# Kernel tuning notes

Hardware: AMD Instinct MI355X
Metric: run time of the kernel (lower is better)

The kernel has to match this reference:

```python
import jax, jax.numpy as jnp
import numpy as np

NEG_SLOPE = 0.01  # nn.LeakyReLU default


def setup_inputs() -> dict:
    key = jax.random.key(0)
    k1, k2, k3, k4, k5 = jax.random.split(key, 5)
    SLI, FEAT, NODE = 8, 64, 20000
    N = SLI * NODE          # 160000 graph nodes
    E = 2_560_000           # avg degree 16
    OUT = 64
    inputs = jax.random.normal(k1, (SLI, FEAT, NODE), dtype=jnp.float32)
    src = jax.random.randint(k2, (E,), 0, N, dtype=jnp.int64)
    dst = jax.random.randint(k3, (E,), 0, N, dtype=jnp.int64)
    # GraphConv params (glorot-ish scale)
    W = jax.random.normal(k4, (FEAT, OUT), dtype=jnp.float32) / np.sqrt(FEAT)
    b = jnp.zeros((OUT,), dtype=jnp.float32)
    return {"inputs": inputs, "W": W, "b": b, "src": src, "dst": dst}


def reference(inputs, W, b, src, dst):
    # inputs: [sli, feat, node] -> [sli*node, feat]  (dropout is eval-mode identity)
    sli, feat, node = inputs.shape
    x = jnp.transpose(inputs, (0, 2, 1)).reshape(-1, feat)
    N = sli * node
    ones = jnp.ones(src.shape, dtype=x.dtype)
    deg_out = jax.ops.segment_sum(ones, src, num_segments=N)  # out-degree of src
    deg_in = jax.ops.segment_sum(ones, dst, num_segments=N)   # in-degree of dst
    norm_src = jnp.where(deg_out > 0, deg_out, 1.0) ** -0.5
    norm_dst = jnp.where(deg_in > 0, deg_in, 1.0) ** -0.5
    # norm='both': scale src feats, sum-aggregate over edges, scale dst
    h = x * norm_src[:, None]
    agg = jax.ops.segment_sum(h[src], dst, num_segments=N)    # [N, feat]
    agg = agg * norm_dst[:, None]
    out = agg @ W + b                                          # [N, out]
    out = jax.nn.leaky_relu(out, NEG_SLOPE)
    # [N, out] -> [sli, node, out] -> [sli, out, node]
    return jnp.transpose(out.reshape(sli, node, -1), (0, 2, 1))
```

## Files before the change

kernel.cpp:

```cpp
#include <hip/hip_runtime.h>
#include <hip/hip_bf16.h>

constexpr int SLI  = 8;
constexpr int FEAT = 64;
constexpr int NODE = 20000;
constexpr int NTOT = SLI * NODE;
constexpr int OUTF = 64;
constexpr int CAP  = 48;
constexpr int NB   = 313;
constexpr int BCAP = 8960;
constexpr int EPB  = 4096;
constexpr int NDST = NTOT / 256;

typedef __attribute__((ext_vector_type(8))) short bf16x8;
typedef __attribute__((ext_vector_type(4))) float f32x4;

static __device__ inline unsigned short f2bf(float x) {
    unsigned u = __float_as_uint(x);
    unsigned r = (u + 0x7fffu + ((u >> 16) & 1u)) >> 16;
    return (unsigned short)r;
}
static __device__ inline float bf2f(unsigned short h) {
    return __uint_as_float((unsigned)h << 16);
}

__global__ __launch_bounds__(256) void k_part(const int* __restrict__ src,
                                              const int* __restrict__ dst,
                                              int* __restrict__ cursor_d,
                                              unsigned* __restrict__ bucket_d,
                                              int* __restrict__ cursor_s,
                                              unsigned short* __restrict__ bucket_s, int E) {
    __shared__ unsigned       svalD[EPB];
    __shared__ unsigned short sbktD[EPB];
    __shared__ unsigned short svalS[EPB];
    __shared__ unsigned short sbktS[EPB];
    __shared__ int histD[NB], loffD[NB], lcurD[NB], baseD[NB];
    __shared__ int histS[NB], loffS[NB], lcurS[NB], baseS[NB];
    __shared__ int goffD[64], goffS[64];
    int t  = threadIdx.x;
    int e0 = blockIdx.x * EPB;
    for (int i = t; i < NB; i += 256) { histD[i] = 0; histS[i] = 0; }
    __syncthreads();
    int myS[16], myD[16];
#pragma unroll
    for (int i = 0; i < 16; ++i) {
        int idx = e0 + i * 256 + t;
        if (idx < E) {
            myS[i] = src[idx];
            myD[i] = dst[idx];
            atomicAdd(&histD[myD[i] >> 9], 1);
            atomicAdd(&histS[myS[i] >> 9], 1);
        } else { myS[i] = -1; myD[i] = -1; }
    }
    __syncthreads();
    int wv = t >> 6, ln = t & 63;
    if (wv == 0) {
        int b0 = ln * 5, s = 0;
#pragma unroll
        for (int j = 0; j < 5; ++j) { int bb = b0 + j; if (bb < NB) s += histD[bb]; }
        int x = s;
        for (int off = 1; off < 64; off <<= 1) {
            int y = __shfl_up(x, off, 64);
            if (ln >= off) x += y;
        }
        goffD[ln] = x - s;
    } else if (wv == 1) {
        int b0 = ln * 5, s = 0;
#pragma unroll
        for (int j = 0; j < 5; ++j) { int bb = b0 + j; if (bb < NB) s += histS[bb]; }
        int x = s;
        for (int off = 1; off < 64; off <<= 1) {
            int y = __shfl_up(x, off, 64);
            if (ln >= off) x += y;
        }
        goffS[ln] = x - s;
    }
    __syncthreads();
    for (int bb = t; bb < NB; bb += 256) {
        int g5 = bb / 5;
        int sD = goffD[g5], sS = goffS[g5];
        for (int k = g5 * 5; k < bb; ++k) { sD += histD[k]; sS += histS[k]; }
        loffD[bb] = sD; lcurD[bb] = sD;
        baseD[bb] = atomicAdd(&cursor_d[bb], histD[bb]);
        loffS[bb] = sS; lcurS[bb] = sS;
        baseS[bb] = atomicAdd(&cursor_s[bb], histS[bb]);
    }
    __syncthreads();
#pragma unroll
    for (int i = 0; i < 16; ++i) {
        if (myD[i] >= 0) {
            int bD = myD[i] >> 9;
            int p  = atomicAdd(&lcurD[bD], 1);
            svalD[p] = ((unsigned)(myD[i] & 511) << 18) | (unsigned)myS[i];
            sbktD[p] = (unsigned short)bD;
            int bS = myS[i] >> 9;
            int q  = atomicAdd(&lcurS[bS], 1);
            svalS[q] = (unsigned short)(myS[i] & 511);
            sbktS[q] = (unsigned short)bS;
        }
    }
    __syncthreads();
    int nval = E - e0; if (nval > EPB) nval = EPB;
    for (int p = t; p < nval; p += 256) {
        int bD = sbktD[p];
        int wi = baseD[bD] + (p - loffD[bD]);
        if (wi < BCAP) bucket_d[(size_t)bD * BCAP + wi] = svalD[p];
        int bS = sbktS[p];
        int wj = baseS[bS] + (p - loffS[bS]);
        if (wj < BCAP) bucket_s[(size_t)bS * BCAP + wj] = svalS[p];
    }
}

__global__ __launch_bounds__(256) void k_fin(const int* __restrict__ cursor_d,
                                             const unsigned* __restrict__ bucket_d,
                                             const int* __restrict__ cursor_s,
                                             const unsigned short* __restrict__ bucket_s,
                                             int* __restrict__ col_ell,
                                             int* __restrict__ deg_in,
                                             int* __restrict__ deg_out) {
    __shared__ char lds[256 * CAP * 4 + 2048];
    int t = threadIdx.x;
    if (blockIdx.x < NDST) {
        int* ell = (int*)lds;
        int* cnt = (int*)(lds + 256 * CAP * 4);
        int blk  = blockIdx.x, b = blk >> 1, half = blk & 1;
        cnt[t] = 0;
        __syncthreads();
        int len = cursor_d[b]; if (len > BCAP) len = BCAP;
        const unsigned* p = bucket_d + (size_t)b * BCAP;
        for (int i = t; i < len; i += 256) {
            unsigned e = p[i];
            int dl = e >> 18;
            if ((dl >> 8) == half) {
                int r = dl & 255;
                int pos = atomicAdd(&cnt[r], 1);
                if (pos < CAP) ell[r * CAP + pos] = (int)(e & 0x3FFFFu);
            }
        }
        __syncthreads();
        int node0 = blk << 8;
        deg_in[node0 + t] = cnt[t];
        size_t gbase = (size_t)node0 * CAP;
        const int4* lsrc = (const int4*)ell;
        int4* gdst = (int4*)(col_ell + gbase);
#pragma unroll
        for (int i = 0; i < 12; ++i)
            gdst[i * 256 + t] = lsrc[i * 256 + t];
    } else {
        int* cnt = (int*)lds;
        int b = blockIdx.x - NDST;
        cnt[t] = 0; cnt[t + 256] = 0;
        __syncthreads();
        int len = cursor_s[b]; if (len > BCAP) len = BCAP;
        const unsigned short* p = bucket_s + (size_t)b * BCAP;
        for (int i = t; i < len; i += 256)
            atomicAdd(&cnt[p[i]], 1);
        __syncthreads();
        int n0 = b << 9;
        if (n0 + t < NTOT)       deg_out[n0 + t] = cnt[t];
        if (n0 + 256 + t < NTOT) deg_out[n0 + 256 + t] = cnt[t + 256];
    }
}

__global__ __launch_bounds__(256) void k_transpose(const float* __restrict__ in,
                                                   const int* __restrict__ deg_out,
                                                   __hip_bfloat16* __restrict__ xs) {
    __shared__ float tile[64][65];
    int sli = blockIdx.y;
    int n0  = blockIdx.x * 64;
    int t   = threadIdx.x;
    int tx  = t & 63;
    int tr  = t >> 6;
    const float* ip = in + (size_t)sli * FEAT * NODE;
#pragma unroll
    for (int i = 0; i < 16; ++i) {
        int f    = tr + i * 4;
        int node = n0 + tx;
        float v  = 0.f;
        if (node < NODE) v = ip[(size_t)f * NODE + node];
        tile[f][tx] = v;
    }
    __syncthreads();
#pragma unroll
    for (int i = 0; i < 16; ++i) {
        int nl   = tr + i * 4;
        int node = n0 + nl;
        if (node < NODE) {
            int n = sli * NODE + node;
            int d = deg_out[n];
            float scale = rsqrtf(d > 0 ? (float)d : 1.f);
            xs[(size_t)n * FEAT + tx] = (__hip_bfloat16)(tile[tx][nl] * scale);
        }
    }
}

__global__ __launch_bounds__(256) void k_agg_gemm(const int* __restrict__ deg_in,
                                                  const int* __restrict__ col_ell,
                                                  const unsigned short* __restrict__ xs,
                                                  const float* __restrict__ W,
                                                  const float* __restrict__ b,
                                                  float* __restrict__ out) {
    __shared__ char lds[27648];
    unsigned short* av_hi = (unsigned short*)lds;
    unsigned short* av_lo = (unsigned short*)(lds + 9216);
    unsigned short* wt    = (unsigned short*)(lds + 18432);
    float (*otile)[65]    = (float(*)[65])lds;

    int t    = threadIdx.x;
    int lane = t & 63;
    int w    = t >> 6;
    int gq   = lane >> 4;
    int fl   = lane & 15;
    int sli  = blockIdx.y;
    int n0   = blockIdx.x * 64;

#pragma unroll
    for (int i = 0; i < 16; ++i) {
        int idx = i * 256 + t;
        int f = idx >> 6, o = idx & 63;
        wt[o * 72 + f] = f2bf(W[idx]);
    }

    int m0 = w * 16;
    for (int ii = 0; ii < 16; ii += 2) {
        int rowA = m0 + ii, rowB = rowA + 1;
        int nodeA = n0 + rowA, nodeB = n0 + rowB;
        int nA = sli * NODE + nodeA, nB = sli * NODE + nodeB;
        int dA = (nodeA < NODE) ? deg_in[nA] : 0;
        int dB = (nodeB < NODE) ? deg_in[nB] : 0;
        int degA = dA < CAP ? dA : CAP;
        int degB = dB < CAP ? dB : CAP;
        int cA = (lane < degA) ? col_ell[(size_t)nA * CAP + lane] : 0;
        int cB = (lane < degB) ? col_ell[(size_t)nB * CAP + lane] : 0;
        float a0 = 0.f, a1 = 0.f, a2 = 0.f, a3 = 0.f;
        float b0 = 0.f, b1 = 0.f, b2 = 0.f, b3 = 0.f;
        int gmax = degA > degB ? degA : degB;
        int groups = (gmax + 3) >> 2;
        for (int j = 0; j < groups; ++j) {
            int idx = 4 * j + gq;
            int sA = __shfl(cA, idx, 64);
            int sB = __shfl(cB, idx, 64);
            uint2 vA = *(const uint2*)(xs + (size_t)sA * 64 + fl * 4);
            uint2 vB = *(const uint2*)(xs + (size_t)sB * 64 + fl * 4);
            if (idx < degA) {
                a0 += __uint_as_float(vA.x << 16);
                a1 += __uint_as_float(vA.x & 0xffff0000u);
                a2 += __uint_as_float(vA.y << 16);
                a3 += __uint_as_float(vA.y & 0xffff0000u);
            }
            if (idx < degB) {
                b0 += __uint_as_float(vB.x << 16);
                b1 += __uint_as_float(vB.x & 0xffff0000u);
                b2 += __uint_as_float(vB.y << 16);
                b3 += __uint_as_float(vB.y & 0xffff0000u);
            }
        }
        a0 += __shfl_xor(a0, 16, 64); a0 += __shfl_xor(a0, 32, 64);
        a1 += __shfl_xor(a1, 16, 64); a1 += __shfl_xor(a1, 32, 64);
        a2 += __shfl_xor(a2, 16, 64); a2 += __shfl_xor(a2, 32, 64);
        a3 += __shfl_xor(a3, 16, 64); a3 += __shfl_xor(a3, 32, 64);
        b0 += __shfl_xor(b0, 16, 64); b0 += __shfl_xor(b0, 32, 64);
        b1 += __shfl_xor(b1, 16, 64); b1 += __shfl_xor(b1, 32, 64);
        b2 += __shfl_xor(b2, 16, 64); b2 += __shfl_xor(b2, 32, 64);
        b3 += __shfl_xor(b3, 16, 64); b3 += __shfl_xor(b3, 32, 64);
        if (gq == 0) {
            float scA = rsqrtf(dA > 0 ? (float)dA : 1.f);
            float scB = rsqrtf(dB > 0 ? (float)dB : 1.f);
            float s0 = a0 * scA, s1 = a1 * scA, s2 = a2 * scA, s3 = a3 * scA;
            float u0 = b0 * scB, u1 = b1 * scB, u2 = b2 * scB, u3 = b3 * scB;
            unsigned short h0 = f2bf(s0), h1 = f2bf(s1), h2 = f2bf(s2), h3 = f2bf(s3);
            uint2 hv, lv;
            hv.x = (unsigned)h0 | ((unsigned)h1 << 16);
            hv.y = (unsigned)h2 | ((unsigned)h3 << 16);
            lv.x = (unsigned)f2bf(s0 - bf2f(h0)) | ((unsigned)f2bf(s1 - bf2f(h1)) << 16);
            lv.y = (unsigned)f2bf(s2 - bf2f(h2)) | ((unsigned)f2bf(s3 - bf2f(h3)) << 16);
            ((uint2*)av_hi)[rowA * 18 + fl] = hv;
            ((uint2*)av_lo)[rowA * 18 + fl] = lv;
            unsigned short g0 = f2bf(u0), g1 = f2bf(u1), g2 = f2bf(u2), g3 = f2bf(u3);
            hv.x = (unsigned)g0 | ((unsigned)g1 << 16);
            hv.y = (unsigned)g2 | ((unsigned)g3 << 16);
            lv.x = (unsigned)f2bf(u0 - bf2f(g0)) | ((unsigned)f2bf(u1 - bf2f(g1)) << 16);
            lv.y = (unsigned)f2bf(u2 - bf2f(g2)) | ((unsigned)f2bf(u3 - bf2f(g3)) << 16);
            ((uint2*)av_hi)[rowB * 18 + fl] = hv;
            ((uint2*)av_lo)[rowB * 18 + fl] = lv;
        }
    }

    __syncthreads();

    int q = lane >> 4, r16 = lane & 15;
    bf16x8 a_hi[2], a_lo[2], bfr[4][2];
#pragma unroll
    for (int ks = 0; ks < 2; ++ks) {
        a_hi[ks] = *(const bf16x8*)(av_hi + (m0 + r16) * 72 + ks * 32 + q * 8);
        a_lo[ks] = *(const bf16x8*)(av_lo + (m0 + r16) * 72 + ks * 32 + q * 8);
    }
#pragma unroll
    for (int nt = 0; nt < 4; ++nt)
#pragma unroll
        for (int ks = 0; ks < 2; ++ks)
            bfr[nt][ks] = *(const bf16x8*)(wt + (nt * 16 + r16) * 72 + ks * 32 + q * 8);

    f32x4 acc4[4];
#pragma unroll
    for (int nt = 0; nt < 4; ++nt) acc4[nt] = (f32x4){0.f, 0.f, 0.f, 0.f};
#pragma unroll
    for (int nt = 0; nt < 4; ++nt)
#pragma unroll
        for (int ks = 0; ks < 2; ++ks) {
            acc4[nt] = __builtin_amdgcn_mfma_f32_16x16x32_bf16(a_hi[ks], bfr[nt][ks], acc4[nt], 0, 0, 0);
            acc4[nt] = __builtin_amdgcn_mfma_f32_16x16x32_bf16(a_lo[ks], bfr[nt][ks], acc4[nt], 0, 0, 0);
        }
    __syncthreads();

#pragma unroll
    for (int nt = 0; nt < 4; ++nt) {
        int oc = nt * 16 + r16;
        float bias = b[oc];
#pragma unroll
        for (int r = 0; r < 4; ++r) {
            float v = acc4[nt][r] + bias;
            v = v > 0.f ? v : 0.01f * v;
            otile[oc][m0 + q * 4 + r] = v;
        }
    }
    __syncthreads();

    const size_t obase = (size_t)sli * OUTF * NODE;
#pragma unroll
    for (int i = 0; i < 16; ++i) {
        int o    = w + i * 4;
        int node = n0 + lane;
        if (node < NODE)
            out[obase + (size_t)o * NODE + node] = otile[o][lane];
    }
}

extern "C" void kernel_launch(void* const* d_in, const int* in_sizes, int n_in,
                              void* d_out, int out_size, void* d_ws, size_t ws_size,
                              hipStream_t stream) {
    const float* inputs = (const float*)d_in[0];
    const float* W      = (const float*)d_in[1];
    const float* b      = (const float*)d_in[2];
    const int*   src    = (const int*)d_in[3];
    const int*   dst    = (const int*)d_in[4];
    float*       out    = (float*)d_out;
    const int E = in_sizes[3];

    char* ws = (char*)d_ws;
    int* deg_out = (int*)ws;
    int* deg_in  = (int*)(ws + (size_t)NTOT * 4);
    int* col_ell = (int*)(ws + (size_t)2 * NTOT * 4);
    char* R      = (char*)col_ell + (size_t)NTOT * CAP * 4;
    unsigned*       bucket_d = (unsigned*)R;
    unsigned short* bucket_s = (unsigned short*)(R + (size_t)NB * BCAP * 4);
    int*            cursors  = (int*)(R + (size_t)NB * BCAP * 6);
    int* cursor_d = cursors;
    int* cursor_s = cursors + NB;
    __hip_bfloat16* xs = (__hip_bfloat16*)R;

    hipMemsetAsync(cursors, 0, (size_t)2 * NB * 4, stream);

    int PB = (E + EPB - 1) / EPB;
    k_part<<<PB, 256, 0, stream>>>(src, dst, cursor_d, bucket_d, cursor_s, bucket_s, E);

    k_fin<<<NDST + NB, 256, 0, stream>>>(cursor_d, bucket_d, cursor_s, bucket_s,
                                         col_ell, deg_in, deg_out);

    dim3 tgrid((NODE + 63) / 64, SLI);
    k_transpose<<<tgrid, 256, 0, stream>>>(inputs, deg_out, xs);

    k_agg_gemm<<<tgrid, 256, 0, stream>>>(deg_in, col_ell,
                                          (const unsigned short*)xs, W, b, out);
}
```

Before: 261.4 us.

## Drop hi/lo bf16 split, widen gather loads, vectorize transpose, pack partition LDS

The aggregation GEMM now uses a single bf16 operand instead of the hi+lo split, which halves the MFMA work and A-tile LDS traffic but loses the extra precision the split provided. The gather loop reads 16 bytes per lane over 8 edges per iteration. Padded lanes point at a zero row at index NTOT (cleared by a memset) instead of using per-edge predicates. The transpose kernel uses float4 loads and packed bf16x2 stores, and the partition kernel merges the src value and bucket into one 32-bit LDS word.

```diff
diff --git a/kernel.cpp b/kernel.cpp
--- a/kernel.cpp
+++ b/kernel.cpp
@@ -20,9 +20,6 @@
     unsigned r = (u + 0x7fffu + ((u >> 16) & 1u)) >> 16;
     return (unsigned short)r;
 }
-static __device__ inline float bf2f(unsigned short h) {
-    return __uint_as_float((unsigned)h << 16);
-}
 
 __global__ __launch_bounds__(256) void k_part(const int* __restrict__ src,
                                               const int* __restrict__ dst,
@@ -32,8 +29,7 @@
                                               unsigned short* __restrict__ bucket_s, int E) {
     __shared__ unsigned       svalD[EPB];
     __shared__ unsigned short sbktD[EPB];
-    __shared__ unsigned short svalS[EPB];
-    __shared__ unsigned short sbktS[EPB];
+    __shared__ unsigned       sS[EPB];
     __shared__ int histD[NB], loffD[NB], lcurD[NB], baseD[NB];
     __shared__ int histS[NB], loffS[NB], lcurS[NB], baseS[NB];
     __shared__ int goffD[64], goffS[64];
@@ -78,11 +74,11 @@
     __syncthreads();
     for (int bb = t; bb < NB; bb += 256) {
         int g5 = bb / 5;
-        int sD = goffD[g5], sS = goffS[g5];
-        for (int k = g5 * 5; k < bb; ++k) { sD += histD[k]; sS += histS[k]; }
+        int sD = goffD[g5], sS2 = goffS[g5];
+        for (int k = g5 * 5; k < bb; ++k) { sD += histD[k]; sS2 += histS[k]; }
         loffD[bb] = sD; lcurD[bb] = sD;
         baseD[bb] = atomicAdd(&cursor_d[bb], histD[bb]);
-        loffS[bb] = sS; lcurS[bb] = sS;
+        loffS[bb] = sS2; lcurS[bb] = sS2;
         baseS[bb] = atomicAdd(&cursor_s[bb], histS[bb]);
     }
     __syncthreads();
@@ -95,8 +91,7 @@
             sbktD[p] = (unsigned short)bD;
             int bS = myS[i] >> 9;
             int q  = atomicAdd(&lcurS[bS], 1);
-            svalS[q] = (unsigned short)(myS[i] & 511);
-            sbktS[q] = (unsigned short)bS;
+            sS[q] = ((unsigned)bS << 9) | (unsigned)(myS[i] & 511);
         }
     }
     __syncthreads();
@@ -105,9 +100,10 @@
         int bD = sbktD[p];
         int wi = baseD[bD] + (p - loffD[bD]);
         if (wi < BCAP) bucket_d[(size_t)bD * BCAP + wi] = svalD[p];
-        int bS = sbktS[p];
+        unsigned vs = sS[p];
+        int bS = vs >> 9;
         int wj = baseS[bS] + (p - loffS[bS]);
-        if (wj < BCAP) bucket_s[(size_t)bS * BCAP + wj] = svalS[p];
+        if (wj < BCAP) bucket_s[(size_t)bS * BCAP + wj] = (unsigned short)(vs & 511);
     }
 }
 
@@ -164,32 +160,39 @@
 
 __global__ __launch_bounds__(256) void k_transpose(const float* __restrict__ in,
                                                    const int* __restrict__ deg_out,
-                                                   __hip_bfloat16* __restrict__ xs) {
+                                                   unsigned short* __restrict__ xs) {
     __shared__ float tile[64][65];
     int sli = blockIdx.y;
     int n0  = blockIdx.x * 64;
     int t   = threadIdx.x;
-    int tx  = t & 63;
-    int tr  = t >> 6;
+    int fx  = t & 15;
+    int fr  = t >> 4;
     const float* ip = in + (size_t)sli * FEAT * NODE;
-#pragma unroll
-    for (int i = 0; i < 16; ++i) {
-        int f    = tr + i * 4;
-        int node = n0 + tx;
-        float v  = 0.f;
-        if (node < NODE) v = ip[(size_t)f * NODE + node];
-        tile[f][tx] = v;
-    }
-    __syncthreads();
-#pragma unroll
-    for (int i = 0; i < 16; ++i) {
-        int nl   = tr + i * 4;
+    int nq = n0 + fx * 4;
+#pragma unroll
+    for (int i = 0; i < 4; ++i) {
+        int f = fr + i * 16;
+        float4 v = {0.f, 0.f, 0.f, 0.f};
+        if (nq < NODE) v = *(const float4*)(ip + (size_t)f * NODE + nq);
+        tile[f][fx * 4 + 0] = v.x;
+        tile[f][fx * 4 + 1] = v.y;
+        tile[f][fx * 4 + 2] = v.z;
+        tile[f][fx * 4 + 3] = v.w;
+    }
+    __syncthreads();
+    int h  = t & 31;
+    int nr = t >> 5;
+#pragma unroll
+    for (int i = 0; i < 8; ++i) {
+        int nl   = nr + i * 8;
         int node = n0 + nl;
         if (node < NODE) {
             int n = sli * NODE + node;
             int d = deg_out[n];
-            float scale = rsqrtf(d > 0 ? (float)d : 1.f);
-            xs[(size_t)n * FEAT + tx] = (__hip_bfloat16)(tile[tx][nl] * scale);
+            float sc = rsqrtf(d > 0 ? (float)d : 1.f);
+            unsigned lo = f2bf(tile[2 * h][nl] * sc);
+            unsigned hi = f2bf(tile[2 * h + 1][nl] * sc);
+            *(unsigned*)(xs + (size_t)n * 64 + 2 * h) = lo | (hi << 16);
         }
     }
 }
@@ -200,17 +203,16 @@
                                                   const float* __restrict__ W,
                                                   const float* __restrict__ b,
                                                   float* __restrict__ out) {
-    __shared__ char lds[27648];
-    unsigned short* av_hi = (unsigned short*)lds;
-    unsigned short* av_lo = (unsigned short*)(lds + 9216);
-    unsigned short* wt    = (unsigned short*)(lds + 18432);
-    float (*otile)[65]    = (float(*)[65])lds;
+    __shared__ char lds[18432];
+    unsigned short* av = (unsigned short*)lds;
+    unsigned short* wt = (unsigned short*)(lds + 9216);
+    float (*otile)[65] = (float(*)[65])lds;
 
     int t    = threadIdx.x;
     int lane = t & 63;
     int w    = t >> 6;
-    int gq   = lane >> 4;
-    int fl   = lane & 15;
+    int g8   = lane >> 3;
+    int f8   = lane & 7;
     int sli  = blockIdx.y;
     int n0   = blockIdx.x * 64;
 
@@ -230,71 +232,68 @@
         int dB = (nodeB < NODE) ? deg_in[nB] : 0;
         int degA = dA < CAP ? dA : CAP;
         int degB = dB < CAP ? dB : CAP;
-        int cA = (lane < degA) ? col_ell[(size_t)nA * CAP + lane] : 0;
-        int cB = (lane < degB) ? col_ell[(size_t)nB * CAP + lane] : 0;
-        float a0 = 0.f, a1 = 0.f, a2 = 0.f, a3 = 0.f;
-        float b0 = 0.f, b1 = 0.f, b2 = 0.f, b3 = 0.f;
+        int cA = (lane < degA) ? col_ell[(size_t)nA * CAP + lane] : NTOT;
+        int cB = (lane < degB) ? col_ell[(size_t)nB * CAP + lane] : NTOT;
+        float accA[8] = {0,0,0,0,0,0,0,0};
+        float accB[8] = {0,0,0,0,0,0,0,0};
         int gmax = degA > degB ? degA : degB;
-        int groups = (gmax + 3) >> 2;
+        int groups = (gmax + 7) >> 3;
         for (int j = 0; j < groups; ++j) {
-            int idx = 4 * j + gq;
+            int idx = 8 * j + g8;
             int sA = __shfl(cA, idx, 64);
             int sB = __shfl(cB, idx, 64);
-            uint2 vA = *(const uint2*)(xs + (size_t)sA * 64 + fl * 4);
-            uint2 vB = *(const uint2*)(xs + (size_t)sB * 64 + fl * 4);
-            if (idx < degA) {
-                a0 += __uint_as_float(vA.x << 16);
-                a1 += __uint_as_float(vA.x & 0xffff0000u);
-                a2 += __uint_as_float(vA.y << 16);
-                a3 += __uint_as_float(vA.y & 0xffff0000u);
-            }
-            if (idx < degB) {
-                b0 += __uint_as_float(vB.x << 16);
-                b1 += __uint_as_float(vB.x & 0xffff0000u);
-                b2 += __uint_as_float(vB.y << 16);
-                b3 += __uint_as_float(vB.y & 0xffff0000u);
-            }
-        }
-        a0 += __shfl_xor(a0, 16, 64); a0 += __shfl_xor(a0, 32, 64);
-        a1 += __shfl_xor(a1, 16, 64); a1 += __shfl_xor(a1, 32, 64);
-        a2 += __shfl_xor(a2, 16, 64); a2 += __shfl_xor(a2, 32, 64);
-        a3 += __shfl_xor(a3, 16, 64); a3 += __shfl_xor(a3, 32, 64);
-        b0 += __shfl_xor(b0, 16, 64); b0 += __shfl_xor(b0, 32, 64);
-        b1 += __shfl_xor(b1, 16, 64); b1 += __shfl_xor(b1, 32, 64);
-        b2 += __shfl_xor(b2, 16, 64); b2 += __shfl_xor(b2, 32, 64);
-        b3 += __shfl_xor(b3, 16, 64); b3 += __shfl_xor(b3, 32, 64);
-        if (gq == 0) {
+            uint4 vA = *(const uint4*)(xs + (size_t)sA * 64 + f8 * 8);
+            uint4 vB = *(const uint4*)(xs + (size_t)sB * 64 + f8 * 8);
+            accA[0] += __uint_as_float(vA.x << 16);
+            accA[1] += __uint_as_float(vA.x & 0xffff0000u);
+            accA[2] += __uint_as_float(vA.y << 16);
+            accA[3] += __uint_as_float(vA.y & 0xffff0000u);
+            accA[4] += __uint_as_float(vA.z << 16);
+            accA[5] += __uint_as_float(vA.z & 0xffff0000u);
+            accA[6] += __uint_as_float(vA.w << 16);
+            accA[7] += __uint_as_float(vA.w & 0xffff0000u);
+            accB[0] += __uint_as_float(vB.x << 16);
+            accB[1] += __uint_as_float(vB.x & 0xffff0000u);
+            accB[2] += __uint_as_float(vB.y << 16);
+            accB[3] += __uint_as_float(vB.y & 0xffff0000u);
+            accB[4] += __uint_as_float(vB.z << 16);
+            accB[5] += __uint_as_float(vB.z & 0xffff0000u);
+            accB[6] += __uint_as_float(vB.w << 16);
+            accB[7] += __uint_as_float(vB.w & 0xffff0000u);
+        }
+#pragma unroll
+        for (int k = 0; k < 8; ++k) {
+            accA[k] += __shfl_xor(accA[k], 8, 64);
+            accA[k] += __shfl_xor(accA[k], 16, 64);
+            accA[k] += __shfl_xor(accA[k], 32, 64);
+            accB[k] += __shfl_xor(accB[k], 8, 64);
+            accB[k] += __shfl_xor(accB[k], 16, 64);
+            accB[k] += __shfl_xor(accB[k], 32, 64);
+        }
+        if (g8 == 0) {
             float scA = rsqrtf(dA > 0 ? (float)dA : 1.f);
             float scB = rsqrtf(dB > 0 ? (float)dB : 1.f);
-            float s0 = a0 * scA, s1 = a1 * scA, s2 = a2 * scA, s3 = a3 * scA;
-            float u0 = b0 * scB, u1 = b1 * scB, u2 = b2 * scB, u3 = b3 * scB;
-            unsigned short h0 = f2bf(s0), h1 = f2bf(s1), h2 = f2bf(s2), h3 = f2bf(s3);
-            uint2 hv, lv;
-            hv.x = (unsigned)h0 | ((unsigned)h1 << 16);
-            hv.y = (unsigned)h2 | ((unsigned)h3 << 16);
-            lv.x = (unsigned)f2bf(s0 - bf2f(h0)) | ((unsigned)f2bf(s1 - bf2f(h1)) << 16);
-            lv.y = (unsigned)f2bf(s2 - bf2f(h2)) | ((unsigned)f2bf(s3 - bf2f(h3)) << 16);
-            ((uint2*)av_hi)[rowA * 18 + fl] = hv;
-            ((uint2*)av_lo)[rowA * 18 + fl] = lv;
-            unsigned short g0 = f2bf(u0), g1 = f2bf(u1), g2 = f2bf(u2), g3 = f2bf(u3);
-            hv.x = (unsigned)g0 | ((unsigned)g1 << 16);
-            hv.y = (unsigned)g2 | ((unsigned)g3 << 16);
-            lv.x = (unsigned)f2bf(u0 - bf2f(g0)) | ((unsigned)f2bf(u1 - bf2f(g1)) << 16);
-            lv.y = (unsigned)f2bf(u2 - bf2f(g2)) | ((unsigned)f2bf(u3 - bf2f(g3)) << 16);
-            ((uint2*)av_hi)[rowB * 18 + fl] = hv;
-            ((uint2*)av_lo)[rowB * 18 + fl] = lv;
+            uint4 hv;
+            hv.x = (unsigned)f2bf(accA[0] * scA) | ((unsigned)f2bf(accA[1] * scA) << 16);
+            hv.y = (unsigned)f2bf(accA[2] * scA) | ((unsigned)f2bf(accA[3] * scA) << 16);
+            hv.z = (unsigned)f2bf(accA[4] * scA) | ((unsigned)f2bf(accA[5] * scA) << 16);
+            hv.w = (unsigned)f2bf(accA[6] * scA) | ((unsigned)f2bf(accA[7] * scA) << 16);
+            ((uint4*)(av + rowA * 72))[f8] = hv;
+            hv.x = (unsigned)f2bf(accB[0] * scB) | ((unsigned)f2bf(accB[1] * scB) << 16);
+            hv.y = (unsigned)f2bf(accB[2] * scB) | ((unsigned)f2bf(accB[3] * scB) << 16);
+            hv.z = (unsigned)f2bf(accB[4] * scB) | ((unsigned)f2bf(accB[5] * scB) << 16);
+            hv.w = (unsigned)f2bf(accB[6] * scB) | ((unsigned)f2bf(accB[7] * scB) << 16);
+            ((uint4*)(av + rowB * 72))[f8] = hv;
         }
     }
 
     __syncthreads();
 
     int q = lane >> 4, r16 = lane & 15;
-    bf16x8 a_hi[2], a_lo[2], bfr[4][2];
-#pragma unroll
-    for (int ks = 0; ks < 2; ++ks) {
-        a_hi[ks] = *(const bf16x8*)(av_hi + (m0 + r16) * 72 + ks * 32 + q * 8);
-        a_lo[ks] = *(const bf16x8*)(av_lo + (m0 + r16) * 72 + ks * 32 + q * 8);
-    }
+    bf16x8 afr[2], bfr[4][2];
+#pragma unroll
+    for (int ks = 0; ks < 2; ++ks)
+        afr[ks] = *(const bf16x8*)(av + (m0 + r16) * 72 + ks * 32 + q * 8);
 #pragma unroll
     for (int nt = 0; nt < 4; ++nt)
 #pragma unroll
@@ -307,10 +306,8 @@
 #pragma unroll
     for (int nt = 0; nt < 4; ++nt)
 #pragma unroll
-        for (int ks = 0; ks < 2; ++ks) {
-            acc4[nt] = __builtin_amdgcn_mfma_f32_16x16x32_bf16(a_hi[ks], bfr[nt][ks], acc4[nt], 0, 0, 0);
-            acc4[nt] = __builtin_amdgcn_mfma_f32_16x16x32_bf16(a_lo[ks], bfr[nt][ks], acc4[nt], 0, 0, 0);
-        }
+        for (int ks = 0; ks < 2; ++ks)
+            acc4[nt] = __builtin_amdgcn_mfma_f32_16x16x32_bf16(afr[ks], bfr[nt][ks], acc4[nt], 0, 0, 0);
     __syncthreads();
 
 #pragma unroll
@@ -357,9 +354,10 @@
     int*            cursors  = (int*)(R + (size_t)NB * BCAP * 6);
     int* cursor_d = cursors;
     int* cursor_s = cursors + NB;
-    __hip_bfloat16* xs = (__hip_bfloat16*)R;
+    unsigned short* xs = (unsigned short*)R;
 
     hipMemsetAsync(cursors, 0, (size_t)2 * NB * 4, stream);
+    hipMemsetAsync(xs + (size_t)NTOT * 64, 0, 64 * sizeof(unsigned short), stream);
 
     int PB = (E + EPB - 1) / EPB;
     k_part<<<PB, 256, 0, stream>>>(src, dst, cursor_d, bucket_d, cursor_s, bucket_s, E);
@@ -370,6 +368,5 @@
     dim3 tgrid((NODE + 63) / 64, SLI);
     k_transpose<<<tgrid, 256, 0, stream>>>(inputs, deg_out, xs);
 
-    k_agg_gemm<<<tgrid, 256, 0, stream>>>(deg_in, col_ell,
-                                          (const unsigned short*)xs, W, b, out);
-}
+    k_agg_gemm<<<tgrid, 256, 0, stream>>>(deg_in, col_ell, xs, W, b, out);
+}
```

After: 241.7 us. -7.5%, faster.
